# Kernel tuning notes

Measured on AMD Instinct MI355X. Metric: run time of the kernel, lower is better.

## Reference

```python
import jax, jax.numpy as jnp
import numpy as np

CHANNELS = 64
K = 3
STRIDE = 1
GROUP_CHANNELS = 2
GROUPS = CHANNELS // GROUP_CHANNELS  # 32
RED = 4
PAD = (K - 1) // 2


def setup_inputs() -> dict:
    key = jax.random.key(0)
    ks = jax.random.split(key, 6)
    x = jax.random.normal(ks[0], (8, CHANNELS, 128, 128), dtype=jnp.float32)
    w1 = jax.random.normal(ks[1], (CHANNELS // RED, CHANNELS), dtype=jnp.float32) * 0.05
    b1 = jax.random.normal(ks[2], (CHANNELS // RED,), dtype=jnp.float32) * 0.05
    prelu_a = jnp.full((1,), 0.25, dtype=jnp.float32)
    w2 = jax.random.normal(ks[3], (K * K * GROUPS, CHANNELS // RED), dtype=jnp.float32) * 0.05
    b2 = jax.random.normal(ks[4], (K * K * GROUPS,), dtype=jnp.float32) * 0.05
    return {"x": x, "w1": w1, "b1": b1, "prelu_a": prelu_a, "w2": w2, "b2": b2}


def reference(x, w1, b1, prelu_a, w2, b2):
    # stride == 1: no avgpool
    # 1x1 conv -> PReLU -> 1x1 conv to generate per-pixel kernels
    t = jnp.einsum('bchw,oc->bohw', x, w1) + b1[None, :, None, None]
    t = jnp.where(t >= 0, t, prelu_a[0] * t)  # PReLU, single shared slope
    weight = jnp.einsum('bchw,oc->bohw', t, w2) + b2[None, :, None, None]
    b, _, h, w = weight.shape
    # (b, groups, 1, k^2, h, w)
    weight = weight.reshape(b, GROUPS, 1, K * K, h, w)
    # unfold: im2col with padding 1, stride 1; channel-major (c, kh, kw) ordering like torch.nn.Unfold
    xp = jnp.pad(x, ((0, 0), (0, 0), (PAD, PAD), (PAD, PAD)))
    patches = jnp.stack(
        [xp[:, :, i:i + h, j:j + w] for i in range(K) for j in range(K)], axis=2
    )  # (b, c, k^2, h, w)
    patches = patches.reshape(b, GROUPS, GROUP_CHANNELS, K * K, h, w)
    out = (weight * patches).sum(axis=3).reshape(b, CHANNELS, h, w)
    return out
```

## Files before the change

### kernel.cpp

```cpp
#include <hip/hip_runtime.h>

#define NPIX (128 * 128)
#define CH 64
#define RMID 16
#define KK 9
#define PLANE_B 65536

typedef float v2f __attribute__((ext_vector_type(2)));

#define ASM_LOAD2(dst, base, voff) \
    asm volatile("global_load_dwordx2 %0, %1, %2" \
                 : "=v"(dst) : "v"((uint32_t)(voff)), "s"(base))

#define VMWAIT(N) do { \
    asm volatile("s_waitcnt vmcnt(" #N ")" ::: "memory"); \
    __builtin_amdgcn_sched_barrier(0); \
} while (0)

#define ISSUE8(B, base, oct) do { \
    const uint32_t c0 = (uint32_t)pb0 + (uint32_t)((oct) * 8) * 65536u; \
    ASM_LOAD2(B##0, base, c0); \
    ASM_LOAD2(B##1, base, c0 + 1u * 65536u); \
    ASM_LOAD2(B##2, base, c0 + 2u * 65536u); \
    ASM_LOAD2(B##3, base, c0 + 3u * 65536u); \
    ASM_LOAD2(B##4, base, c0 + 4u * 65536u); \
    ASM_LOAD2(B##5, base, c0 + 5u * 65536u); \
    ASM_LOAD2(B##6, base, c0 + 6u * 65536u); \
    ASM_LOAD2(B##7, base, c0 + 7u * 65536u); \
} while (0)

#define FMA8(xvreg, ch) do { \
    _Pragma("unroll") \
    for (int r = 0; r < RMID; ++r) { \
        const float w = w1[r * CH + (ch)]; \
        v2f wv; wv.x = w; wv.y = w; \
        t2[r] = __builtin_elementwise_fma(wv, (xvreg), t2[r]); \
    } \
} while (0)

#define CONSUME8(B, oct) do { \
    FMA8(B##0, (oct) * 8 + 0); \
    FMA8(B##1, (oct) * 8 + 1); \
    FMA8(B##2, (oct) * 8 + 2); \
    FMA8(B##3, (oct) * 8 + 3); \
    FMA8(B##4, (oct) * 8 + 4); \
    FMA8(B##5, (oct) * 8 + 5); \
    FMA8(B##6, (oct) * 8 + 6); \
    FMA8(B##7, (oct) * 8 + 7); \
} while (0)

#define ISSUE_TAPS(B, gg) do { \
    const uint32_t q0 = (uint32_t)pb0 + (uint32_t)(2 * (gg)) * 65536u; \
    const uint32_t q1 = q0 + 65536u; \
    ASM_LOAD2(B##A0, xbc, q0 + (uint32_t)ro0); \
    ASM_LOAD2(B##A1, xbc, q0); \
    ASM_LOAD2(B##A2, xbc, q0 + (uint32_t)ro2); \
    ASM_LOAD2(B##E0, xbc, q1 + (uint32_t)ro0); \
    ASM_LOAD2(B##E1, xbc, q1); \
    ASM_LOAD2(B##E2, xbc, q1 + (uint32_t)ro2); \
} while (0)

#define PRELU_T2() do { \
    const float a = prelu_a[0]; \
    v2f av; av.x = a; av.y = a; \
    v2f z;  z.x = 0.f; z.y = 0.f; \
    _Pragma("unroll") \
    for (int r = 0; r < RMID; ++r) { \
        const v2f pos = __builtin_elementwise_max(t2[r], z); \
        const v2f neg = __builtin_elementwise_min(t2[r], z); \
        t2[r] = __builtin_elementwise_fma(av, neg, pos); \
    } \
} while (0)

#define CONV1_LADDER() do { \
    VMWAIT(8);  CONSUME8(xA, 0); ISSUE8(xA, xbc, 2); \
    VMWAIT(8);  CONSUME8(xB, 1); ISSUE8(xB, xbc, 3); \
    VMWAIT(8);  CONSUME8(xA, 2); ISSUE8(xA, xbc, 4); \
    VMWAIT(8);  CONSUME8(xB, 3); ISSUE8(xB, xbc, 5); \
    VMWAIT(8);  CONSUME8(xA, 4); ISSUE8(xA, xbc, 6); \
    VMWAIT(8);  CONSUME8(xB, 5); ISSUE8(xB, xbc, 7); \
    VMWAIT(8);  CONSUME8(xA, 6); \
    VMWAIT(0);  CONSUME8(xB, 7); \
} while (0)

__device__ __forceinline__ void group_tail(
    int g, v2f tA0, v2f tA1, v2f tA2, v2f tE0, v2f tE1, v2f tE2,
    float mL, float mR, v2f rm0v, v2f rm2v,
    const v2f (&t2)[RMID], const float* __restrict__ w2,
    const float* __restrict__ b2, char* obc, int pb0)
{
    const v2f A0 = tA0 * rm0v;
    const v2f A1 = tA1;
    const v2f A2 = tA2 * rm2v;
    const v2f E0 = tE0 * rm0v;
    const v2f E1 = tE1;
    const v2f E2 = tE2 * rm2v;

    const float lA0 = __shfl_up(A0.y, 1), rA0 = __shfl_down(A0.x, 1);
    const float lA1 = __shfl_up(A1.y, 1), rA1 = __shfl_down(A1.x, 1);
    const float lA2 = __shfl_up(A2.y, 1), rA2 = __shfl_down(A2.x, 1);
    const float lE0 = __shfl_up(E0.y, 1), rE0 = __shfl_down(E0.x, 1);
    const float lE1 = __shfl_up(E1.y, 1), rE1 = __shfl_down(E1.x, 1);
    const float lE2 = __shfl_up(E2.y, 1), rE2 = __shfl_down(E2.x, 1);

    v2f oA; oA.x = 0.f; oA.y = 0.f;
    v2f oB = oA;
#pragma unroll
    for (int k = 0; k < KK; ++k) {
        const float* w2r = w2 + (g * KK + k) * RMID;
        const float bb = b2[g * KK + k];
        v2f acc; acc.x = bb; acc.y = bb;
#pragma unroll
        for (int r = 0; r < RMID; ++r) {
            const float w = w2r[r];
            v2f wv; wv.x = w; wv.y = w;
            acc = __builtin_elementwise_fma(wv, t2[r], acc);
        }
        if (k == 0 || k == 3 || k == 6) acc.x *= mL;
        if (k == 2 || k == 5 || k == 8) acc.y *= mR;

        const v2f Ar = (k < 3) ? A0 : (k < 6) ? A1 : A2;
        const v2f Er = (k < 3) ? E0 : (k < 6) ? E1 : E2;
        const float lA = (k < 3) ? lA0 : (k < 6) ? lA1 : lA2;
        const float rA = (k < 3) ? rA0 : (k < 6) ? rA1 : rA2;
        const float lE = (k < 3) ? lE0 : (k < 6) ? lE1 : lE2;
        const float rE = (k < 3) ? rE0 : (k < 6) ? rE1 : rE2;

        v2f tpA, tpE;
        if (k % 3 == 0)      { tpA.x = lA;   tpA.y = Ar.x;
                               tpE.x = lE;   tpE.y = Er.x; }
        else if (k % 3 == 1) { tpA = Ar;     tpE = Er;     }
        else                 { tpA.x = Ar.y; tpA.y = rA;
                               tpE.x = Er.y; tpE.y = rE;   }
        oA = __builtin_elementwise_fma(acc, tpA, oA);
        oB = __builtin_elementwise_fma(acc, tpE, oB);
    }

    __builtin_nontemporal_store(oA, (v2f*)(obc + (size_t)(2 * g)     * PLANE_B + pb0));
    __builtin_nontemporal_store(oB, (v2f*)(obc + (size_t)(2 * g + 1) * PLANE_B + pb0));
}

#define GSTEP(Bcur, Bnext, gcur) do { \
    ISSUE_TAPS(Bnext, (gcur) + 1); VMWAIT(6); \
    group_tail((gcur), Bcur##A0, Bcur##A1, Bcur##A2, Bcur##E0, Bcur##E1, Bcur##E2, \
               mL, mR, rm0v, rm2v, t2, w2, b2, obc, pb0); \
} while (0)

__global__ __launch_bounds__(256, 2) void invol_fused(
    const float* __restrict__ x,
    const float* __restrict__ w1,
    const float* __restrict__ b1,
    const float* __restrict__ prelu_a,
    const float* __restrict__ w2,
    const float* __restrict__ b2,
    float* __restrict__ out)
{
    const int c    = threadIdx.x & 63;
    const int rsub = threadIdx.x >> 6;

    const int L     = blockIdx.x;
    const int bq    = L & 7;
    const int go    = (L >> 3) & 1;
    const int strip = L >> 4;

    const int hq  = 4 * strip + rsub;
    const int p0  = hq * 128 + 2 * c;
    const int pb0 = 4 * p0;

    const char* xbc = (const char*)(x + (size_t)bq * CH * NPIX);

    const float rm0 = (hq > 0)   ? 1.f : 0.f;
    const float rm2 = (hq < 127) ? 1.f : 0.f;
    const float mL  = (c > 0)    ? 1.f : 0.f;
    const float mR  = (c < 63)   ? 1.f : 0.f;
    const int   ro0 = (hq > 0)   ? -512 : 0;
    const int   ro2 = (hq < 127) ?  512 : 0;

    v2f xA0, xA1, xA2, xA3, xA4, xA5, xA6, xA7;
    v2f xB0, xB1, xB2, xB3, xB4, xB5, xB6, xB7;
    v2f taA0, taA1, taA2, taE0, taE1, taE2;
    v2f tbA0, tbA1, tbA2, tbE0, tbE1, tbE2;

    const int g0 = 16 * go;
    ISSUE_TAPS(ta, g0 + 0);
    ISSUE8(xA, xbc, 0);
    ISSUE8(xB, xbc, 1);

    v2f t2[RMID];
#pragma unroll
    for (int r = 0; r < RMID; ++r) {
        const float b = b1[r];
        t2[r].x = b; t2[r].y = b;
    }

    CONV1_LADDER();
    PRELU_T2();

    v2f rm0v; rm0v.x = rm0; rm0v.y = rm0;
    v2f rm2v; rm2v.x = rm2; rm2v.y = rm2;
    char* obc = (char*)(out + (size_t)bq * CH * NPIX);

    GSTEP(ta, tb, g0 + 0);
    GSTEP(tb, ta, g0 + 1);
    GSTEP(ta, tb, g0 + 2);
    GSTEP(tb, ta, g0 + 3);
    GSTEP(ta, tb, g0 + 4);
    GSTEP(tb, ta, g0 + 5);
    GSTEP(ta, tb, g0 + 6);
    GSTEP(tb, ta, g0 + 7);
    GSTEP(ta, tb, g0 + 8);
    GSTEP(tb, ta, g0 + 9);
    GSTEP(ta, tb, g0 + 10);
    GSTEP(tb, ta, g0 + 11);
    GSTEP(ta, tb, g0 + 12);
    GSTEP(tb, ta, g0 + 13);
    GSTEP(ta, tb, g0 + 14);
    VMWAIT(2);
    group_tail(g0 + 15, tbA0, tbA1, tbA2, tbE0, tbE1, tbE2,
               mL, mR, rm0v, rm2v, t2, w2, b2, obc, pb0);
}

extern "C" void kernel_launch(void* const* d_in, const int* in_sizes, int n_in,
                              void* d_out, int out_size, void* d_ws, size_t ws_size,
                              hipStream_t stream)
{
    const float* x  = (const float*)d_in[0];
    const float* w1 = (const float*)d_in[1];
    const float* b1 = (const float*)d_in[2];
    const float* pa = (const float*)d_in[3];
    const float* w2 = (const float*)d_in[4];
    const float* b2 = (const float*)d_in[5];
    float* out = (float*)d_out;

    hipLaunchKernelGGL(invol_fused, dim3(512), dim3(256), 0, stream,
                       x, w1, b1, pa, w2, b2, out);
}
```

Before: 122.2 us.

## Split group work four ways and load right-neighbor taps instead of shuffling

New measurement: 113.8 us. 6.9% less time.

```diff
diff --git a/kernel.cpp b/kernel.cpp
--- a/kernel.cpp
+++ b/kernel.cpp
@@ -10,6 +10,10 @@
 
 #define ASM_LOAD2(dst, base, voff) \
     asm volatile("global_load_dwordx2 %0, %1, %2" \
+                 : "=v"(dst) : "v"((uint32_t)(voff)), "s"(base))
+
+#define ASM_LOAD1(dst, base, voff) \
+    asm volatile("global_load_dword %0, %1, %2" \
                  : "=v"(dst) : "v"((uint32_t)(voff)), "s"(base))
 
 #define VMWAIT(N) do { \
@@ -58,6 +62,12 @@
     ASM_LOAD2(B##E0, xbc, q1 + (uint32_t)ro0); \
     ASM_LOAD2(B##E1, xbc, q1); \
     ASM_LOAD2(B##E2, xbc, q1 + (uint32_t)ro2); \
+    ASM_LOAD1(B##rA0, xbc, q0 + (uint32_t)ro0 + rsel); \
+    ASM_LOAD1(B##rA1, xbc, q0 + rsel); \
+    ASM_LOAD1(B##rA2, xbc, q0 + (uint32_t)ro2 + rsel); \
+    ASM_LOAD1(B##rE0, xbc, q1 + (uint32_t)ro0 + rsel); \
+    ASM_LOAD1(B##rE1, xbc, q1 + rsel); \
+    ASM_LOAD1(B##rE2, xbc, q1 + (uint32_t)ro2 + rsel); \
 } while (0)
 
 #define PRELU_T2() do { \
@@ -85,7 +95,8 @@
 
 __device__ __forceinline__ void group_tail(
     int g, v2f tA0, v2f tA1, v2f tA2, v2f tE0, v2f tE1, v2f tE2,
-    float mL, float mR, v2f rm0v, v2f rm2v,
+    float rA0, float rA1, float rA2, float rE0, float rE1, float rE2,
+    float mL, float mR, float rm0, float rm2, v2f rm0v, v2f rm2v,
     const v2f (&t2)[RMID], const float* __restrict__ w2,
     const float* __restrict__ b2, char* obc, int pb0)
 {
@@ -95,13 +106,15 @@
     const v2f E0 = tE0 * rm0v;
     const v2f E1 = tE1;
     const v2f E2 = tE2 * rm2v;
-
-    const float lA0 = __shfl_up(A0.y, 1), rA0 = __shfl_down(A0.x, 1);
-    const float lA1 = __shfl_up(A1.y, 1), rA1 = __shfl_down(A1.x, 1);
-    const float lA2 = __shfl_up(A2.y, 1), rA2 = __shfl_down(A2.x, 1);
-    const float lE0 = __shfl_up(E0.y, 1), rE0 = __shfl_down(E0.x, 1);
-    const float lE1 = __shfl_up(E1.y, 1), rE1 = __shfl_down(E1.x, 1);
-    const float lE2 = __shfl_up(E2.y, 1), rE2 = __shfl_down(E2.x, 1);
+    rA0 *= rm0;  rA2 *= rm2;
+    rE0 *= rm0;  rE2 *= rm2;
+
+    const float lA0 = __shfl_up(A0.y, 1);
+    const float lA1 = __shfl_up(A1.y, 1);
+    const float lA2 = __shfl_up(A2.y, 1);
+    const float lE0 = __shfl_up(E0.y, 1);
+    const float lE1 = __shfl_up(E1.y, 1);
+    const float lE2 = __shfl_up(E2.y, 1);
 
     v2f oA; oA.x = 0.f; oA.y = 0.f;
     v2f oB = oA;
@@ -141,9 +154,10 @@
 }
 
 #define GSTEP(Bcur, Bnext, gcur) do { \
-    ISSUE_TAPS(Bnext, (gcur) + 1); VMWAIT(6); \
+    ISSUE_TAPS(Bnext, (gcur) + 1); VMWAIT(12); \
     group_tail((gcur), Bcur##A0, Bcur##A1, Bcur##A2, Bcur##E0, Bcur##E1, Bcur##E2, \
-               mL, mR, rm0v, rm2v, t2, w2, b2, obc, pb0); \
+               Bcur##rA0, Bcur##rA1, Bcur##rA2, Bcur##rE0, Bcur##rE1, Bcur##rE2, \
+               mL, mR, rm0, rm2, rm0v, rm2v, t2, w2, b2, obc, pb0); \
 } while (0)
 
 __global__ __launch_bounds__(256, 2) void invol_fused(
@@ -160,8 +174,8 @@
 
     const int L     = blockIdx.x;
     const int bq    = L & 7;
-    const int go    = (L >> 3) & 1;
-    const int strip = L >> 4;
+    const int go    = (L >> 3) & 3;
+    const int strip = L >> 5;
 
     const int hq  = 4 * strip + rsub;
     const int p0  = hq * 128 + 2 * c;
@@ -175,13 +189,16 @@
     const float mR  = (c < 63)   ? 1.f : 0.f;
     const int   ro0 = (hq > 0)   ? -512 : 0;
     const int   ro2 = (hq < 127) ?  512 : 0;
+    const uint32_t rsel = (c < 63) ? 8u : 0u;
 
     v2f xA0, xA1, xA2, xA3, xA4, xA5, xA6, xA7;
     v2f xB0, xB1, xB2, xB3, xB4, xB5, xB6, xB7;
     v2f taA0, taA1, taA2, taE0, taE1, taE2;
     v2f tbA0, tbA1, tbA2, tbE0, tbE1, tbE2;
-
-    const int g0 = 16 * go;
+    float tarA0, tarA1, tarA2, tarE0, tarE1, tarE2;
+    float tbrA0, tbrA1, tbrA2, tbrE0, tbrE1, tbrE2;
+
+    const int g0 = 8 * go;
     ISSUE_TAPS(ta, g0 + 0);
     ISSUE8(xA, xbc, 0);
     ISSUE8(xB, xbc, 1);
@@ -207,17 +224,10 @@
     GSTEP(ta, tb, g0 + 4);
     GSTEP(tb, ta, g0 + 5);
     GSTEP(ta, tb, g0 + 6);
-    GSTEP(tb, ta, g0 + 7);
-    GSTEP(ta, tb, g0 + 8);
-    GSTEP(tb, ta, g0 + 9);
-    GSTEP(ta, tb, g0 + 10);
-    GSTEP(tb, ta, g0 + 11);
-    GSTEP(ta, tb, g0 + 12);
-    GSTEP(tb, ta, g0 + 13);
-    GSTEP(ta, tb, g0 + 14);
     VMWAIT(2);
-    group_tail(g0 + 15, tbA0, tbA1, tbA2, tbE0, tbE1, tbE2,
-               mL, mR, rm0v, rm2v, t2, w2, b2, obc, pb0);
+    group_tail(g0 + 7, tbA0, tbA1, tbA2, tbE0, tbE1, tbE2,
+               tbrA0, tbrA1, tbrA2, tbrE0, tbrE1, tbrE2,
+               mL, mR, rm0, rm2, rm0v, rm2v, t2, w2, b2, obc, pb0);
 }
 
 extern "C" void kernel_launch(void* const* d_in, const int* in_sizes, int n_in,
@@ -232,6 +242,6 @@
     const float* b2 = (const float*)d_in[5];
     float* out = (float*)d_out;
 
-    hipLaunchKernelGGL(invol_fused, dim3(512), dim3(256), 0, stream,
+    hipLaunchKernelGGL(invol_fused, dim3(1024), dim3(256), 0, stream,
                        x, w1, b1, pa, w2, b2, out);
 }
```

## Split groups across four blocks per strip and deepen conv1 load pipeline

Applied to the files above, without the earlier changes.

New measurement: 115.8 us. 1.06x faster.

```diff
diff --git a/kernel.cpp b/kernel.cpp
--- a/kernel.cpp
+++ b/kernel.cpp
@@ -72,13 +72,13 @@
     } \
 } while (0)
 
-#define CONV1_LADDER() do { \
-    VMWAIT(8);  CONSUME8(xA, 0); ISSUE8(xA, xbc, 2); \
-    VMWAIT(8);  CONSUME8(xB, 1); ISSUE8(xB, xbc, 3); \
-    VMWAIT(8);  CONSUME8(xA, 2); ISSUE8(xA, xbc, 4); \
-    VMWAIT(8);  CONSUME8(xB, 3); ISSUE8(xB, xbc, 5); \
-    VMWAIT(8);  CONSUME8(xA, 4); ISSUE8(xA, xbc, 6); \
-    VMWAIT(8);  CONSUME8(xB, 5); ISSUE8(xB, xbc, 7); \
+#define CONV1_LADDER3() do { \
+    VMWAIT(16); CONSUME8(xA, 0); ISSUE8(xA, xbc, 3); \
+    VMWAIT(16); CONSUME8(xB, 1); ISSUE8(xB, xbc, 4); \
+    VMWAIT(16); CONSUME8(xC, 2); ISSUE8(xC, xbc, 5); \
+    VMWAIT(16); CONSUME8(xA, 3); ISSUE8(xA, xbc, 6); \
+    VMWAIT(16); CONSUME8(xB, 4); ISSUE8(xB, xbc, 7); \
+    VMWAIT(16); CONSUME8(xC, 5); \
     VMWAIT(8);  CONSUME8(xA, 6); \
     VMWAIT(0);  CONSUME8(xB, 7); \
 } while (0)
@@ -140,12 +140,6 @@
     __builtin_nontemporal_store(oB, (v2f*)(obc + (size_t)(2 * g + 1) * PLANE_B + pb0));
 }
 
-#define GSTEP(Bcur, Bnext, gcur) do { \
-    ISSUE_TAPS(Bnext, (gcur) + 1); VMWAIT(6); \
-    group_tail((gcur), Bcur##A0, Bcur##A1, Bcur##A2, Bcur##E0, Bcur##E1, Bcur##E2, \
-               mL, mR, rm0v, rm2v, t2, w2, b2, obc, pb0); \
-} while (0)
-
 __global__ __launch_bounds__(256, 2) void invol_fused(
     const float* __restrict__ x,
     const float* __restrict__ w1,
@@ -160,8 +154,8 @@
 
     const int L     = blockIdx.x;
     const int bq    = L & 7;
-    const int go    = (L >> 3) & 1;
-    const int strip = L >> 4;
+    const int go    = (L >> 3) & 3;
+    const int strip = L >> 5;
 
     const int hq  = 4 * strip + rsub;
     const int p0  = hq * 128 + 2 * c;
@@ -178,13 +172,15 @@
 
     v2f xA0, xA1, xA2, xA3, xA4, xA5, xA6, xA7;
     v2f xB0, xB1, xB2, xB3, xB4, xB5, xB6, xB7;
+    v2f xC0, xC1, xC2, xC3, xC4, xC5, xC6, xC7;
     v2f taA0, taA1, taA2, taE0, taE1, taE2;
     v2f tbA0, tbA1, tbA2, tbE0, tbE1, tbE2;
 
-    const int g0 = 16 * go;
+    const int g0 = 8 * go;
     ISSUE_TAPS(ta, g0 + 0);
     ISSUE8(xA, xbc, 0);
     ISSUE8(xB, xbc, 1);
+    ISSUE8(xC, xbc, 2);
 
     v2f t2[RMID];
 #pragma unroll
@@ -193,31 +189,29 @@
         t2[r].x = b; t2[r].y = b;
     }
 
-    CONV1_LADDER();
+    CONV1_LADDER3();
     PRELU_T2();
 
     v2f rm0v; rm0v.x = rm0; rm0v.y = rm0;
     v2f rm2v; rm2v.x = rm2; rm2v.y = rm2;
     char* obc = (char*)(out + (size_t)bq * CH * NPIX);
 
-    GSTEP(ta, tb, g0 + 0);
-    GSTEP(tb, ta, g0 + 1);
-    GSTEP(ta, tb, g0 + 2);
-    GSTEP(tb, ta, g0 + 3);
-    GSTEP(ta, tb, g0 + 4);
-    GSTEP(tb, ta, g0 + 5);
-    GSTEP(ta, tb, g0 + 6);
-    GSTEP(tb, ta, g0 + 7);
-    GSTEP(ta, tb, g0 + 8);
-    GSTEP(tb, ta, g0 + 9);
-    GSTEP(ta, tb, g0 + 10);
-    GSTEP(tb, ta, g0 + 11);
-    GSTEP(ta, tb, g0 + 12);
-    GSTEP(tb, ta, g0 + 13);
-    GSTEP(ta, tb, g0 + 14);
+    ISSUE_TAPS(tb, g0 + 1); VMWAIT(6);
+    group_tail(g0 + 0, taA0, taA1, taA2, taE0, taE1, taE2, mL, mR, rm0v, rm2v, t2, w2, b2, obc, pb0);
+    ISSUE_TAPS(ta, g0 + 2); VMWAIT(6);
+    group_tail(g0 + 1, tbA0, tbA1, tbA2, tbE0, tbE1, tbE2, mL, mR, rm0v, rm2v, t2, w2, b2, obc, pb0);
+    ISSUE_TAPS(tb, g0 + 3); VMWAIT(6);
+    group_tail(g0 + 2, taA0, taA1, taA2, taE0, taE1, taE2, mL, mR, rm0v, rm2v, t2, w2, b2, obc, pb0);
+    ISSUE_TAPS(ta, g0 + 4); VMWAIT(6);
+    group_tail(g0 + 3, tbA0, tbA1, tbA2, tbE0, tbE1, tbE2, mL, mR, rm0v, rm2v, t2, w2, b2, obc, pb0);
+    ISSUE_TAPS(tb, g0 + 5); VMWAIT(6);
+    group_tail(g0 + 4, taA0, taA1, taA2, taE0, taE1, taE2, mL, mR, rm0v, rm2v, t2, w2, b2, obc, pb0);
+    ISSUE_TAPS(ta, g0 + 6); VMWAIT(6);
+    group_tail(g0 + 5, tbA0, tbA1, tbA2, tbE0, tbE1, tbE2, mL, mR, rm0v, rm2v, t2, w2, b2, obc, pb0);
+    ISSUE_TAPS(tb, g0 + 7); VMWAIT(6);
+    group_tail(g0 + 6, taA0, taA1, taA2, taE0, taE1, taE2, mL, mR, rm0v, rm2v, t2, w2, b2, obc, pb0);
     VMWAIT(2);
-    group_tail(g0 + 15, tbA0, tbA1, tbA2, tbE0, tbE1, tbE2,
-               mL, mR, rm0v, rm2v, t2, w2, b2, obc, pb0);
+    group_tail(g0 + 7, tbA0, tbA1, tbA2, tbE0, tbE1, tbE2, mL, mR, rm0v, rm2v, t2, w2, b2, obc, pb0);
 }
 
 extern "C" void kernel_launch(void* const* d_in, const int* in_sizes, int n_in,
@@ -232,6 +226,6 @@
     const float* b2 = (const float*)d_in[5];
     float* out = (float*)d_out;
 
-    hipLaunchKernelGGL(invol_fused, dim3(512), dim3(256), 0, stream,
+    hipLaunchKernelGGL(invol_fused, dim3(1024), dim3(256), 0, stream,
                        x, w1, b1, pa, w2, b2, out);
 }
```
